# Optimization experiments

Hardware: AMD Instinct MI355X
Metric: run time of the kernel (lower is better)

Reference implementation:

```python
import jax, jax.numpy as jnp
import numpy as np

CAT_SIZES = [31360, 6807, 18, 94]
TOTAL = int(sum(CAT_SIZES))          # 38279
EMB = 128
N_FIELDS = len(CAT_SIZES)
D_IN = N_FIELDS * EMB                # 512 (num_features is empty)
MLP_DIMS = [2048, 1024, 512]
B = 16384
OFFSETS = np.concatenate([[0], np.cumsum(CAT_SIZES)[:-1]]).astype(np.int32)


def setup_inputs() -> dict:
    key = jax.random.key(0)
    ks = jax.random.split(key, 20)
    # x holds raw per-field category ids stored as float32 (as the torch model expects)
    cols = [jax.random.randint(ks[i], (B,), 0, s) for i, s in enumerate(CAT_SIZES)]
    x = jnp.stack(cols, axis=1).astype(jnp.float32)

    bias = jnp.zeros((1,), jnp.float32)
    fc = jax.random.uniform(ks[4], (TOTAL, 1), dtype=jnp.float32)          # nn.Parameter(torch.rand)
    emb_table = jax.random.normal(ks[5], (TOTAL, EMB), dtype=jnp.float32)  # nn.Embedding default N(0,1)

    dims = [D_IN] + MLP_DIMS + [1]
    params = {}
    for i in range(len(dims) - 1):
        fan_in = dims[i]
        bound = 1.0 / np.sqrt(fan_in)
        params[f"W{i+1}"] = jax.random.uniform(ks[6 + 2 * i], (dims[i], dims[i + 1]), jnp.float32, -bound, bound)
        params[f"b{i+1}"] = jax.random.uniform(ks[7 + 2 * i], (dims[i + 1],), jnp.float32, -bound, bound)

    return dict(x=x, bias=bias, fc=fc, emb_table=emb_table, **params)


def reference(x, bias, fc, emb_table, W1, b1, W2, b2, W3, b3, W4, b4):
    cat = x.astype(jnp.int32)                       # [B, F] raw per-field ids
    b = cat.shape[0]

    # embedding lookup with RAW (un-offset) ids, faithful to the original code
    embed_x = emb_table[cat].reshape(b, -1)          # [B, F*EMB]

    # one_hot(offset ids) @ fc  ==  sum_f fc[offset ids]  (offset ranges disjoint)
    gidx = cat + jnp.asarray(OFFSETS)                # [B, F] global ids
    lin = jnp.sum(fc[gidx, 0], axis=1)               # [B]
    fm_y = bias + lin                                # [B]

    # FM term: embed_x is 2-D, so sum over dim=1 collapses features;
    # the keepdim sum over dim=-1 then collapses the BATCH dim to shape (1,)
    # (a quirk of the original code that we reproduce exactly)
    square_of_sum = jnp.sum(embed_x, axis=1) ** 2    # [B]
    sum_of_square = jnp.sum(embed_x ** 2, axis=1)    # [B]
    fm_y = fm_y + 0.5 * jnp.sum(square_of_sum - sum_of_square, axis=-1, keepdims=True)  # [B]
    fm_y = fm_y[:, None]                             # [B,1]

    # MLP (eval mode: dropout is identity)
    h = embed_x
    for W, bb in ((W1, b1), (W2, b2), (W3, b3)):
        h = jax.nn.relu(h @ W + bb)
    mlp_y = h @ W4 + b4                              # [B,1]

    return jax.nn.sigmoid(fm_y + mlp_y)              # [B,1]
```

## Files before the change

kernel.cpp:

```cpp
#include <hip/hip_runtime.h>
#include <hip/hip_fp8.h>
#include <cstdint>


typedef float f32x4 __attribute__((ext_vector_type(4)));
typedef int i32x4 __attribute__((ext_vector_type(4)));
typedef int i32x8 __attribute__((ext_vector_type(8)));

#define GLOAD16(gptr, lptr)                                                \
  __builtin_amdgcn_global_load_lds(                                        \
      (const __attribute__((address_space(1))) void*)(gptr),               \
      (__attribute__((address_space(3))) void*)(lptr), 16, 0, 0)

__device__ inline uint32_t f2fp4(float v) {
  uint32_t s = (__float_as_uint(v) >> 31) << 3;
  float a = fabsf(v);
  uint32_t m;
  if (a < 0.25f) m = 0;
  else if (a < 0.75f) m = 1;
  else if (a < 1.25f) m = 2;
  else if (a < 1.75f) m = 3;
  else if (a < 2.5f)  m = 4;
  else if (a < 3.5f)  m = 5;
  else if (a < 5.0f)  m = 6;
  else m = 7;
  return s | m;
}
__device__ inline float fp82f(uint8_t b) {
  __hip_fp8_e4m3 t;
  t.__x = b;
  return (float)t;
}

static constexpr size_t OFF_LIN  = 0;
static constexpr size_t OFF_PART = 65536;
static constexpr size_t OFF_S    = 81920;
static constexpr size_t OFF_EMB  = 131072;
static constexpr size_t OFF_H1   = OFF_EMB + 8388608ull;
static constexpr size_t OFF_H2   = OFF_H1 + 33554432ull;
static constexpr size_t OFF_H3   = OFF_H2 + 16777216ull;
static constexpr size_t OFF_W1T  = OFF_H3 + 8388608ull;
static constexpr size_t OFF_W2T  = OFF_W1T + 524288ull;
static constexpr size_t OFF_W3T  = OFF_W2T + 1048576ull;

__global__ void prep(const float* __restrict__ W1, const float* __restrict__ W2,
                     const float* __restrict__ W3, uint8_t* __restrict__ W1T,
                     uint8_t* __restrict__ W2T, uint8_t* __restrict__ W3T,
                     const float* __restrict__ x, const float* __restrict__ fc,
                     const float* __restrict__ emb, uint8_t* __restrict__ ebf,
                     float* __restrict__ lin, float* __restrict__ partials) {
  __shared__ __align__(16) float smem[32 * 33];
  int blk = blockIdx.x;
  int tid = threadIdx.x;
  if (blk < 3584) {
    const float* W;
    uint8_t* WT;
    int K, N, bx, by;
    if (blk < 1024) {
      W = W1; WT = W1T; K = 512; N = 2048; bx = blk & 63; by = blk >> 6;
    } else if (blk < 3072) {
      int t = blk - 1024;
      W = W2; WT = W2T; K = 2048; N = 1024; bx = t & 31; by = t >> 5;
    } else {
      int t = blk - 3072;
      W = W3; WT = W3T; K = 1024; N = 512; bx = t & 15; by = t >> 4;
    }
    int tx = tid & 31, ty = tid >> 5;
    int n0 = bx * 32, k0 = by * 32;
#pragma unroll
    for (int i = ty; i < 32; i += 8)
      smem[i * 33 + tx] = W[(size_t)(k0 + i) * N + n0 + tx];
    __syncthreads();
    if (tx < 16) {
#pragma unroll
      for (int i = ty; i < 32; i += 8) {
        uint32_t lo = f2fp4(smem[(2 * tx) * 33 + i] * 128.f);
        uint32_t hi = f2fp4(smem[(2 * tx + 1) * 33 + i] * 128.f);
        WT[(size_t)(n0 + i) * (K >> 1) + (k0 >> 1) + tx] =
            (uint8_t)(lo | (hi << 4));
      }
    }
  } else {
    int gb = blk - 3584;
    int wv = tid >> 6, lane = tid & 63;
    int b = gb * 4 + wv;
    int f = lane >> 4;
    int idx = (int)x[b * 4 + f];
    const float* row = emb + (size_t)idx * 128 + (lane & 15) * 8;
    float4 v0 = ((const float4*)row)[0];
    float4 v1 = ((const float4*)row)[1];
    float s = v0.x + v0.y + v0.z + v0.w + v1.x + v1.y + v1.z + v1.w;
    float q = v0.x * v0.x + v0.y * v0.y + v0.z * v0.z + v0.w * v0.w +
              v1.x * v1.x + v1.y * v1.y + v1.z * v1.z + v1.w * v1.w;

    int lo = 0, hi = 0;
    lo = __builtin_amdgcn_cvt_pk_fp8_f32(v0.x, v0.y, lo, false);
    lo = __builtin_amdgcn_cvt_pk_fp8_f32(v0.z, v0.w, lo, true);
    hi = __builtin_amdgcn_cvt_pk_fp8_f32(v1.x, v1.y, hi, false);
    hi = __builtin_amdgcn_cvt_pk_fp8_f32(v1.z, v1.w, hi, true);
    int2 pk = make_int2(lo, hi);
    *(int2*)(ebf + (size_t)b * 512 + lane * 8) = pk;

    float lp = 0.f;
    if ((lane & 15) == 0) {
      int off = (f == 1) ? 31360 : (f == 2) ? 38167 : (f == 3) ? 38185 : 0;
      lp = fc[idx + off];
    }
#pragma unroll
    for (int m = 32; m; m >>= 1) {
      s += __shfl_xor(s, m);
      q += __shfl_xor(q, m);
      lp += __shfl_xor(lp, m);
    }
    float* pt = smem;
    if (lane == 0) {
      lin[b] = lp;
      pt[wv] = s * s - q;
    }
    __syncthreads();
    if (tid == 0) partials[gb] = pt[0] + pt[1] + pt[2] + pt[3];
  }
}

__global__ void reduce_partials(const float* __restrict__ p,
                                float* __restrict__ S) {
  int tid = threadIdx.x;
  float v = 0.f;
  for (int i = tid; i < 4096; i += 256) v += p[i];
#pragma unroll
  for (int m = 32; m; m >>= 1) v += __shfl_xor(v, m);
  __shared__ float ps[4];
  if ((tid & 63) == 0) ps[tid >> 6] = v;
  __syncthreads();
  if (tid == 0) S[0] = ps[0] + ps[1] + ps[2] + ps[3];
}

__global__ __launch_bounds__(256) void gemm_mx_relu(
    const uint8_t* __restrict__ A, const uint8_t* __restrict__ BT,
    const float* __restrict__ bias, uint8_t* __restrict__ C, int K, int N,
    int GX) {
  __shared__ __align__(16) uint8_t As[128][256];
  __shared__ __align__(16) uint8_t Bs[128][128];
  int bid = blockIdx.x;
  int by = (bid & 7) + ((bid >> 3) / GX) * 8;
  int bx = (bid >> 3) & (GX - 1);
  int tid = threadIdx.x;
  int wv = tid >> 6, lane = tid & 63;
  int m0 = by * 128, n0 = bx * 128;
  int mw = (wv >> 1) * 64, nw = (wv & 1) * 64;
  int ml = lane & 15, kg = lane >> 4;
  int Kb2 = K >> 1;
  int arow = lane >> 4;
  int brow = lane >> 3;
  int bcol = ((lane & 7) ^ brow) * 16;

  f32x4 acc[4][4];
#pragma unroll
  for (int i = 0; i < 4; ++i)
#pragma unroll
    for (int j = 0; j < 4; ++j) acc[i][j] = (f32x4){0.f, 0.f, 0.f, 0.f};

  for (int kt = 0; kt < K; kt += 256) {
#pragma unroll
    for (int r = 0; r < 8; ++r) {
      int g = r * 4 + wv;
      int trow = 4 * g + arow;
      int acol = ((lane & 15) ^ (trow & 15)) * 16;
      const uint8_t* ga = A + (size_t)(m0 + trow) * K + kt + acol;
      GLOAD16(ga, &As[4 * g][0]);
    }
#pragma unroll
    for (int r = 0; r < 4; ++r) {
      int g = r * 4 + wv;
      const uint8_t* gb =
          BT + (size_t)(n0 + 8 * g + brow) * Kb2 + (kt >> 1) + bcol;
      GLOAD16(gb, &Bs[8 * g][0]);
    }
    __syncthreads();

    i32x4 z = (i32x4){0, 0, 0, 0};
#pragma unroll
    for (int j = 0; j < 2; ++j) {
      int c0 = 8 * j + 2 * kg;
      int pa0 = (c0 ^ ml) * 16;
      int pa1 = ((c0 + 1) ^ ml) * 16;
      int pb = ((4 * j + kg) ^ (ml & 7)) * 16;
      i32x8 af[4], bfr[4];
#pragma unroll
      for (int t = 0; t < 4; ++t) {
        int ra = mw + t * 16 + ml;
        i32x4 a0 = *(const i32x4*)&As[ra][pa0];
        i32x4 a1 = *(const i32x4*)&As[ra][pa1];
        af[t] = __builtin_shufflevector(a0, a1, 0, 1, 2, 3, 4, 5, 6, 7);
        i32x4 vb = *(const i32x4*)&Bs[nw + t * 16 + ml][pb];
        bfr[t] = __builtin_shufflevector(vb, z, 0, 1, 2, 3, 4, 5, 6, 7);
      }
#pragma unroll
      for (int mt = 0; mt < 4; ++mt)
#pragma unroll
        for (int nt = 0; nt < 4; ++nt)
          acc[mt][nt] = __builtin_amdgcn_mfma_scale_f32_16x16x128_f8f6f4(
              af[mt], bfr[nt], acc[mt][nt],
               0,  4,
              0, 0x7F7F7F7F,
              0, 0x78787878);
    }
    __syncthreads();
  }

  int rbase = kg * 4;
#pragma unroll
  for (int nt = 0; nt < 4; ++nt) {
    int col = n0 + nw + nt * 16 + ml;
    float bv = bias[col];
#pragma unroll
    for (int mt = 0; mt < 4; ++mt) {
      int row = m0 + mw + mt * 16 + rbase;
      float v0 = acc[mt][nt][0] + bv, v1 = acc[mt][nt][1] + bv;
      float v2 = acc[mt][nt][2] + bv, v3 = acc[mt][nt][3] + bv;
      v0 = v0 > 0.f ? v0 : 0.f;
      v1 = v1 > 0.f ? v1 : 0.f;
      v2 = v2 > 0.f ? v2 : 0.f;
      v3 = v3 > 0.f ? v3 : 0.f;
      int w01 = __builtin_amdgcn_cvt_pk_fp8_f32(v0, v1, 0, false);
      int w23 = __builtin_amdgcn_cvt_pk_fp8_f32(v2, v3, 0, false);
      C[(size_t)(row + 0) * N + col] = (uint8_t)(w01 & 0xFF);
      C[(size_t)(row + 1) * N + col] = (uint8_t)((w01 >> 8) & 0xFF);
      C[(size_t)(row + 2) * N + col] = (uint8_t)(w23 & 0xFF);
      C[(size_t)(row + 3) * N + col] = (uint8_t)((w23 >> 8) & 0xFF);
    }
  }
}

__global__ void mlp_out_sigmoid(const uint8_t* __restrict__ h3,
                                const float* __restrict__ W4,
                                const float* __restrict__ b4,
                                const float* __restrict__ bias,
                                const float* __restrict__ lin,
                                const float* __restrict__ S,
                                float* __restrict__ out) {
  int tid = threadIdx.x;
  int wv = tid >> 6, lane = tid & 63;
  int b = blockIdx.x * 4 + wv;
  uint64_t pk = *(const uint64_t*)(h3 + (size_t)b * 512 + lane * 8);
  const float* wp = W4 + lane * 8;
  float4 w0 = ((const float4*)wp)[0];
  float4 w1 = ((const float4*)wp)[1];
  float wf[8] = {w0.x, w0.y, w0.z, w0.w, w1.x, w1.y, w1.z, w1.w};
  float acc = 0.f;
#pragma unroll
  for (int j = 0; j < 8; ++j)
    acc += fp82f((uint8_t)(pk >> (8 * j))) * wf[j];
#pragma unroll
  for (int m = 32; m; m >>= 1) acc += __shfl_xor(acc, m);
  if (lane == 0) {
    float z = acc + b4[0] + bias[0] + lin[b] + 0.5f * S[0];
    out[b] = 1.f / (1.f + expf(-z));
  }
}

extern "C" void kernel_launch(void* const* d_in, const int* in_sizes, int n_in,
                              void* d_out, int out_size, void* d_ws,
                              size_t ws_size, hipStream_t stream) {
  const float* x    = (const float*)d_in[0];
  const float* bias = (const float*)d_in[1];
  const float* fc   = (const float*)d_in[2];
  const float* emb  = (const float*)d_in[3];
  const float* W1   = (const float*)d_in[4];
  const float* b1   = (const float*)d_in[5];
  const float* W2   = (const float*)d_in[6];
  const float* b2   = (const float*)d_in[7];
  const float* W3   = (const float*)d_in[8];
  const float* b3   = (const float*)d_in[9];
  const float* W4   = (const float*)d_in[10];
  const float* b4   = (const float*)d_in[11];
  float* out = (float*)d_out;

  char* ws = (char*)d_ws;
  float* lin    = (float*)(ws + OFF_LIN);
  float* part   = (float*)(ws + OFF_PART);
  float* Sp     = (float*)(ws + OFF_S);
  uint8_t* EMBb = (uint8_t*)(ws + OFF_EMB);
  uint8_t* H1   = (uint8_t*)(ws + OFF_H1);
  uint8_t* H2   = (uint8_t*)(ws + OFF_H2);
  uint8_t* H3   = (uint8_t*)(ws + OFF_H3);
  uint8_t* W1T  = (uint8_t*)(ws + OFF_W1T);
  uint8_t* W2T  = (uint8_t*)(ws + OFF_W2T);
  uint8_t* W3T  = (uint8_t*)(ws + OFF_W3T);

  prep<<<7680, 256, 0, stream>>>(W1, W2, W3, W1T, W2T, W3T, x, fc, emb, EMBb,
                                 lin, part);
  reduce_partials<<<1, 256, 0, stream>>>(part, Sp);

  gemm_mx_relu<<<2048, 256, 0, stream>>>(EMBb, W1T, b1, H1, 512, 2048, 16);
  gemm_mx_relu<<<1024, 256, 0, stream>>>(H1, W2T, b2, H2, 2048, 1024, 8);
  gemm_mx_relu<<<512, 256, 0, stream>>>(H2, W3T, b3, H3, 1024, 512, 4);

  mlp_out_sigmoid<<<4096, 256, 0, stream>>>(H3, W4, b4, bias, lin, Sp, out);
}
```

Before: 181.0 us.

## Prefetch GEMM tiles into registers to overlap global loads with MFMA

Replaces direct global-to-LDS async loads with register prefetching. The next K-tile is loaded into registers while the current tile is computed, then written to LDS with an XOR swizzle. Launch bounds now request two blocks per SM. The aim is to hide global memory latency behind the MX-FP8/FP4 MFMA work. In exchange it uses more VGPRs (12 i32x4 prefetch registers), which may compete with the occupancy hint.

```diff
diff --git a/kernel.cpp b/kernel.cpp
--- a/kernel.cpp
+++ b/kernel.cpp
@@ -6,11 +6,6 @@
 typedef float f32x4 __attribute__((ext_vector_type(4)));
 typedef int i32x4 __attribute__((ext_vector_type(4)));
 typedef int i32x8 __attribute__((ext_vector_type(8)));
-
-#define GLOAD16(gptr, lptr)                                                \
-  __builtin_amdgcn_global_load_lds(                                        \
-      (const __attribute__((address_space(1))) void*)(gptr),               \
-      (__attribute__((address_space(3))) void*)(lptr), 16, 0, 0)
 
 __device__ inline uint32_t f2fp4(float v) {
   uint32_t s = (__float_as_uint(v) >> 31) << 3;
@@ -135,7 +130,7 @@
   if (tid == 0) S[0] = ps[0] + ps[1] + ps[2] + ps[3];
 }
 
-__global__ __launch_bounds__(256) void gemm_mx_relu(
+__global__ __launch_bounds__(256, 2) void gemm_mx_relu(
     const uint8_t* __restrict__ A, const uint8_t* __restrict__ BT,
     const float* __restrict__ bias, uint8_t* __restrict__ C, int K, int N,
     int GX) {
@@ -150,9 +145,10 @@
   int mw = (wv >> 1) * 64, nw = (wv & 1) * 64;
   int ml = lane & 15, kg = lane >> 4;
   int Kb2 = K >> 1;
-  int arow = lane >> 4;
-  int brow = lane >> 3;
-  int bcol = ((lane & 7) ^ brow) * 16;
+  int al = lane & 15, arow = lane >> 4;
+  int acol = (al ^ (4 * wv + arow)) * 16;
+  int bl = lane & 7, brow = lane >> 3;
+  int bcol = (bl ^ brow) * 16;
 
   f32x4 acc[4][4];
 #pragma unroll
@@ -160,23 +156,37 @@
 #pragma unroll
     for (int j = 0; j < 4; ++j) acc[i][j] = (f32x4){0.f, 0.f, 0.f, 0.f};
 
+  i32x4 pa[8], pb[4];
+#pragma unroll
+  for (int r = 0; r < 8; ++r)
+    pa[r] = *(const i32x4*)(A + (size_t)(m0 + 16 * r + 4 * wv + arow) * K +
+                            acol);
+#pragma unroll
+  for (int r = 0; r < 4; ++r)
+    pb[r] = *(const i32x4*)(BT + (size_t)(n0 + 32 * r + 8 * wv + brow) * Kb2 +
+                            bcol);
+
   for (int kt = 0; kt < K; kt += 256) {
 #pragma unroll
-    for (int r = 0; r < 8; ++r) {
-      int g = r * 4 + wv;
-      int trow = 4 * g + arow;
-      int acol = ((lane & 15) ^ (trow & 15)) * 16;
-      const uint8_t* ga = A + (size_t)(m0 + trow) * K + kt + acol;
-      GLOAD16(ga, &As[4 * g][0]);
-    }
-#pragma unroll
-    for (int r = 0; r < 4; ++r) {
-      int g = r * 4 + wv;
-      const uint8_t* gb =
-          BT + (size_t)(n0 + 8 * g + brow) * Kb2 + (kt >> 1) + bcol;
-      GLOAD16(gb, &Bs[8 * g][0]);
-    }
+    for (int r = 0; r < 8; ++r)
+      *(i32x4*)&As[16 * r + 4 * wv + arow][al * 16] = pa[r];
+#pragma unroll
+    for (int r = 0; r < 4; ++r)
+      *(i32x4*)&Bs[32 * r + 8 * wv + brow][bl * 16] = pb[r];
     __syncthreads();
+
+    if (kt + 256 < K) {
+#pragma unroll
+      for (int r = 0; r < 8; ++r)
+        pa[r] = *(const i32x4*)(A +
+                                (size_t)(m0 + 16 * r + 4 * wv + arow) * K +
+                                kt + 256 + acol);
+#pragma unroll
+      for (int r = 0; r < 4; ++r)
+        pb[r] = *(const i32x4*)(BT +
+                                (size_t)(n0 + 32 * r + 8 * wv + brow) * Kb2 +
+                                ((kt + 256) >> 1) + bcol);
+    }
 
     i32x4 z = (i32x4){0, 0, 0, 0};
 #pragma unroll
@@ -184,7 +194,7 @@
       int c0 = 8 * j + 2 * kg;
       int pa0 = (c0 ^ ml) * 16;
       int pa1 = ((c0 + 1) ^ ml) * 16;
-      int pb = ((4 * j + kg) ^ (ml & 7)) * 16;
+      int pbo = ((4 * j + kg) ^ (ml & 7)) * 16;
       i32x8 af[4], bfr[4];
 #pragma unroll
       for (int t = 0; t < 4; ++t) {
@@ -192,7 +202,7 @@
         i32x4 a0 = *(const i32x4*)&As[ra][pa0];
         i32x4 a1 = *(const i32x4*)&As[ra][pa1];
         af[t] = __builtin_shufflevector(a0, a1, 0, 1, 2, 3, 4, 5, 6, 7);
-        i32x4 vb = *(const i32x4*)&Bs[nw + t * 16 + ml][pb];
+        i32x4 vb = *(const i32x4*)&Bs[nw + t * 16 + ml][pbo];
         bfr[t] = __builtin_shufflevector(vb, z, 0, 1, 2, 3, 4, 5, 6, 7);
       }
 #pragma unroll
```

After: 185.5 us. 1.02x slower.

## Fuse final W4 dot product into third GEMM epilogue with atomic accumulation

Applied to the files above, without the earlier changes.

The third GEMM no longer writes an fp8 H3 activation that a separate kernel reads back. Its epilogue now applies bias and ReLU, multiplies by W4, reduces across lanes and atomically adds each row's partial dot into a float buffer. That buffer is zeroed in reduce_partials, and a small final kernel applies the sigmoid. This drops the H3 round trip and its fp8 quantization, at the cost of float atomics from the four column blocks and non-deterministic summation order.

```diff
diff --git a/kernel.cpp b/kernel.cpp
--- a/kernel.cpp
+++ b/kernel.cpp
@@ -26,20 +26,15 @@
   else m = 7;
   return s | m;
 }
-__device__ inline float fp82f(uint8_t b) {
-  __hip_fp8_e4m3 t;
-  t.__x = b;
-  return (float)t;
-}
 
 static constexpr size_t OFF_LIN  = 0;
 static constexpr size_t OFF_PART = 65536;
 static constexpr size_t OFF_S    = 81920;
-static constexpr size_t OFF_EMB  = 131072;
+static constexpr size_t OFF_ACC  = 98304;
+static constexpr size_t OFF_EMB  = 262144;
 static constexpr size_t OFF_H1   = OFF_EMB + 8388608ull;
 static constexpr size_t OFF_H2   = OFF_H1 + 33554432ull;
-static constexpr size_t OFF_H3   = OFF_H2 + 16777216ull;
-static constexpr size_t OFF_W1T  = OFF_H3 + 8388608ull;
+static constexpr size_t OFF_W1T  = OFF_H2 + 16777216ull;
 static constexpr size_t OFF_W2T  = OFF_W1T + 524288ull;
 static constexpr size_t OFF_W3T  = OFF_W2T + 1048576ull;
 
@@ -123,7 +118,8 @@
 }
 
 __global__ void reduce_partials(const float* __restrict__ p,
-                                float* __restrict__ S) {
+                                float* __restrict__ S,
+                                float* __restrict__ dotacc) {
   int tid = threadIdx.x;
   float v = 0.f;
   for (int i = tid; i < 4096; i += 256) v += p[i];
@@ -133,6 +129,8 @@
   if ((tid & 63) == 0) ps[tid >> 6] = v;
   __syncthreads();
   if (tid == 0) S[0] = ps[0] + ps[1] + ps[2] + ps[3];
+  float4 z4 = make_float4(0.f, 0.f, 0.f, 0.f);
+  for (int i = tid; i < 4096; i += 256) ((float4*)dotacc)[i] = z4;
 }
 
 __global__ __launch_bounds__(256) void gemm_mx_relu(
@@ -202,8 +200,7 @@
           acc[mt][nt] = __builtin_amdgcn_mfma_scale_f32_16x16x128_f8f6f4(
               af[mt], bfr[nt], acc[mt][nt],
                0,  4,
-              0, 0x7F7F7F7F,
-              0, 0x78787878);
+              0, 0x7F7F7F7F, 0, 0x78787878);
     }
     __syncthreads();
   }
@@ -232,31 +229,113 @@
   }
 }
 
-__global__ void mlp_out_sigmoid(const uint8_t* __restrict__ h3,
-                                const float* __restrict__ W4,
-                                const float* __restrict__ b4,
-                                const float* __restrict__ bias,
-                                const float* __restrict__ lin,
-                                const float* __restrict__ S,
-                                float* __restrict__ out) {
+__global__ __launch_bounds__(256) void gemm_mx_dot(
+    const uint8_t* __restrict__ A, const uint8_t* __restrict__ BT,
+    const float* __restrict__ bias, const float* __restrict__ W4,
+    float* __restrict__ dotacc, int K, int N, int GX) {
+  __shared__ __align__(16) uint8_t As[128][256];
+  __shared__ __align__(16) uint8_t Bs[128][128];
+  int bid = blockIdx.x;
+  int by = (bid & 7) + ((bid >> 3) / GX) * 8;
+  int bx = (bid >> 3) & (GX - 1);
   int tid = threadIdx.x;
   int wv = tid >> 6, lane = tid & 63;
-  int b = blockIdx.x * 4 + wv;
-  uint64_t pk = *(const uint64_t*)(h3 + (size_t)b * 512 + lane * 8);
-  const float* wp = W4 + lane * 8;
-  float4 w0 = ((const float4*)wp)[0];
-  float4 w1 = ((const float4*)wp)[1];
-  float wf[8] = {w0.x, w0.y, w0.z, w0.w, w1.x, w1.y, w1.z, w1.w};
-  float acc = 0.f;
-#pragma unroll
-  for (int j = 0; j < 8; ++j)
-    acc += fp82f((uint8_t)(pk >> (8 * j))) * wf[j];
-#pragma unroll
-  for (int m = 32; m; m >>= 1) acc += __shfl_xor(acc, m);
-  if (lane == 0) {
-    float z = acc + b4[0] + bias[0] + lin[b] + 0.5f * S[0];
-    out[b] = 1.f / (1.f + expf(-z));
-  }
+  int m0 = by * 128, n0 = bx * 128;
+  int mw = (wv >> 1) * 64, nw = (wv & 1) * 64;
+  int ml = lane & 15, kg = lane >> 4;
+  int Kb2 = K >> 1;
+  int arow = lane >> 4;
+  int brow = lane >> 3;
+  int bcol = ((lane & 7) ^ brow) * 16;
+
+  f32x4 acc[4][4];
+#pragma unroll
+  for (int i = 0; i < 4; ++i)
+#pragma unroll
+    for (int j = 0; j < 4; ++j) acc[i][j] = (f32x4){0.f, 0.f, 0.f, 0.f};
+
+  for (int kt = 0; kt < K; kt += 256) {
+#pragma unroll
+    for (int r = 0; r < 8; ++r) {
+      int g = r * 4 + wv;
+      int trow = 4 * g + arow;
+      int acol = ((lane & 15) ^ (trow & 15)) * 16;
+      const uint8_t* ga = A + (size_t)(m0 + trow) * K + kt + acol;
+      GLOAD16(ga, &As[4 * g][0]);
+    }
+#pragma unroll
+    for (int r = 0; r < 4; ++r) {
+      int g = r * 4 + wv;
+      const uint8_t* gb =
+          BT + (size_t)(n0 + 8 * g + brow) * Kb2 + (kt >> 1) + bcol;
+      GLOAD16(gb, &Bs[8 * g][0]);
+    }
+    __syncthreads();
+
+    i32x4 z = (i32x4){0, 0, 0, 0};
+#pragma unroll
+    for (int j = 0; j < 2; ++j) {
+      int c0 = 8 * j + 2 * kg;
+      int pa0 = (c0 ^ ml) * 16;
+      int pa1 = ((c0 + 1) ^ ml) * 16;
+      int pb = ((4 * j + kg) ^ (ml & 7)) * 16;
+      i32x8 af[4], bfr[4];
+#pragma unroll
+      for (int t = 0; t < 4; ++t) {
+        int ra = mw + t * 16 + ml;
+        i32x4 a0 = *(const i32x4*)&As[ra][pa0];
+        i32x4 a1 = *(const i32x4*)&As[ra][pa1];
+        af[t] = __builtin_shufflevector(a0, a1, 0, 1, 2, 3, 4, 5, 6, 7);
+        i32x4 vb = *(const i32x4*)&Bs[nw + t * 16 + ml][pb];
+        bfr[t] = __builtin_shufflevector(vb, z, 0, 1, 2, 3, 4, 5, 6, 7);
+      }
+#pragma unroll
+      for (int mt = 0; mt < 4; ++mt)
+#pragma unroll
+        for (int nt = 0; nt < 4; ++nt)
+          acc[mt][nt] = __builtin_amdgcn_mfma_scale_f32_16x16x128_f8f6f4(
+              af[mt], bfr[nt], acc[mt][nt],
+              0, 4, 0, 0x7F7F7F7F, 0, 0x78787878);
+    }
+    __syncthreads();
+  }
+
+  float bv[4], w4v[4];
+#pragma unroll
+  for (int nt = 0; nt < 4; ++nt) {
+    int col = n0 + nw + nt * 16 + ml;
+    bv[nt] = bias[col];
+    w4v[nt] = W4[col];
+  }
+  int rbase = kg * 4;
+#pragma unroll
+  for (int mt = 0; mt < 4; ++mt) {
+#pragma unroll
+    for (int r = 0; r < 4; ++r) {
+      float p = 0.f;
+#pragma unroll
+      for (int nt = 0; nt < 4; ++nt) {
+        float v = acc[mt][nt][r] + bv[nt];
+        v = v > 0.f ? v : 0.f;
+        p += v * w4v[nt];
+      }
+#pragma unroll
+      for (int m = 1; m < 16; m <<= 1) p += __shfl_xor(p, m);
+      if (ml == 0)
+        atomicAdd(&dotacc[m0 + mw + mt * 16 + rbase + r], p);
+    }
+  }
+}
+
+__global__ void final_out(const float* __restrict__ dotacc,
+                          const float* __restrict__ lin,
+                          const float* __restrict__ S,
+                          const float* __restrict__ bias,
+                          const float* __restrict__ b4,
+                          float* __restrict__ out) {
+  int i = blockIdx.x * 256 + threadIdx.x;
+  float z = dotacc[i] + b4[0] + bias[0] + lin[i] + 0.5f * S[0];
+  out[i] = 1.f / (1.f + expf(-z));
 }
 
 extern "C" void kernel_launch(void* const* d_in, const int* in_sizes, int n_in,
@@ -280,21 +359,21 @@
   float* lin    = (float*)(ws + OFF_LIN);
   float* part   = (float*)(ws + OFF_PART);
   float* Sp     = (float*)(ws + OFF_S);
+  float* dacc   = (float*)(ws + OFF_ACC);
   uint8_t* EMBb = (uint8_t*)(ws + OFF_EMB);
   uint8_t* H1   = (uint8_t*)(ws + OFF_H1);
   uint8_t* H2   = (uint8_t*)(ws + OFF_H2);
-  uint8_t* H3   = (uint8_t*)(ws + OFF_H3);
   uint8_t* W1T  = (uint8_t*)(ws + OFF_W1T);
   uint8_t* W2T  = (uint8_t*)(ws + OFF_W2T);
   uint8_t* W3T  = (uint8_t*)(ws + OFF_W3T);
 
   prep<<<7680, 256, 0, stream>>>(W1, W2, W3, W1T, W2T, W3T, x, fc, emb, EMBb,
                                  lin, part);
-  reduce_partials<<<1, 256, 0, stream>>>(part, Sp);
+  reduce_partials<<<1, 256, 0, stream>>>(part, Sp, dacc);
 
   gemm_mx_relu<<<2048, 256, 0, stream>>>(EMBb, W1T, b1, H1, 512, 2048, 16);
   gemm_mx_relu<<<1024, 256, 0, stream>>>(H1, W2T, b2, H2, 2048, 1024, 8);
-  gemm_mx_relu<<<512, 256, 0, stream>>>(H2, W3T, b3, H3, 1024, 512, 4);
-
-  mlp_out_sigmoid<<<4096, 256, 0, stream>>>(H3, W4, b4, bias, lin, Sp, out);
-}
+  gemm_mx_dot<<<512, 256, 0, stream>>>(H2, W3T, b3, W4, dacc, 1024, 512, 4);
+
+  final_out<<<64, 256, 0, stream>>>(dacc, lin, Sp, bias, b4, out);
+}
```

Measured after the change: 174.8 us. -3.4%, faster.
